# Optimization experiments

Measured on AMD Instinct MI355X. Metric: run time of the kernel, lower is better.

The kernel has to match this reference:

```python
import jax, jax.numpy as jnp
import numpy as np

DIM = 1024
NUM_HEADS = 16
HEAD_DIM = DIM // NUM_HEADS
MAX_LEN = 2048
ROPE_BASE = 10000.0


def _rope_tables(n, d, base=ROPE_BASE):
    inv_freq = 1.0 / (base ** (np.arange(0, d, 2, dtype=np.float32) / d))  # [d/2]
    t = np.arange(n, dtype=np.float32)
    freqs = np.outer(t, inv_freq)  # [n, d/2]
    return jnp.asarray(np.cos(freqs)), jnp.asarray(np.sin(freqs))


def _apply_rotary(x, cos, sin):
    # x: [B, H, N, D]; pairs are consecutive elements (2i, 2i+1)
    xe = x[..., 0::2]
    xo = x[..., 1::2]
    # cos/sin: [N, D/2] -> broadcast over B, H
    oe = xe * cos - xo * sin
    oo = xe * sin + xo * cos
    return jnp.stack([oe, oo], axis=-1).reshape(x.shape)


def setup_inputs() -> dict:
    key = jax.random.key(0)
    ks = jax.random.split(key, 11)
    B, T, S = 4, 2048, 2048
    sc = 1.0 / np.sqrt(DIM)
    inp = {
        "query": jax.random.normal(ks[0], (B, T, DIM), jnp.float32),
        "key": jax.random.normal(ks[1], (B, S, DIM), jnp.float32),
        "value": jax.random.normal(ks[2], (B, S, DIM), jnp.float32),
        "Wq": jax.random.normal(ks[3], (DIM, DIM), jnp.float32) * sc,
        "bq": jnp.zeros((DIM,), jnp.float32),
        "Wk": jax.random.normal(ks[4], (DIM, DIM), jnp.float32) * sc,
        "bk": jnp.zeros((DIM,), jnp.float32),
        "Wv": jax.random.normal(ks[5], (DIM, DIM), jnp.float32) * sc,
        "bv": jnp.zeros((DIM,), jnp.float32),
        "Wo": jax.random.normal(ks[6], (DIM, DIM), jnp.float32) * sc,
        "bo": jnp.zeros((DIM,), jnp.float32),
    }
    return inp


def reference(query, key, value, Wq, bq, Wk, bk, Wv, bv, Wo, bo):
    B, T, C = query.shape
    S = key.shape[1]
    H, D = NUM_HEADS, HEAD_DIM
    scale = D ** -0.5

    q = (query @ Wq + bq).reshape(B, T, H, D).transpose(0, 2, 1, 3)  # [B,H,T,D]
    k = (key @ Wk + bk).reshape(B, S, H, D).transpose(0, 2, 1, 3)    # [B,H,S,D]
    v = (value @ Wv + bv).reshape(B, S, H, D).transpose(0, 2, 1, 3)  # [B,H,S,D]

    cos, sin = _rope_tables(max(T, S), D)
    q = _apply_rotary(q, cos[:T], sin[:T])
    k = _apply_rotary(k, cos[:S], sin[:S])

    scores = jnp.einsum("bhtd,bhsd->bhts", q, k) * scale  # [B,H,T,S]
    causal = jnp.tril(jnp.ones((T, S), bool))
    scores = jnp.where(causal[None, None], scores, -jnp.inf)
    att = jax.nn.softmax(scores, axis=-1)

    out = jnp.einsum("bhts,bhsd->bhtd", att, v)  # [B,H,T,D]
    out = out.transpose(0, 2, 1, 3).reshape(B, T, C)
    return out @ Wo + bo
```

## Files before the change

kernel.cpp:

```cpp
#include <hip/hip_runtime.h>
#include <cstdint>
#include <math.h>

typedef __bf16 bf16_t;
typedef __bf16 bf16x8 __attribute__((ext_vector_type(8)));
typedef __bf16 bf16x4 __attribute__((ext_vector_type(4)));
typedef float f32x4 __attribute__((ext_vector_type(4)));

#define MFMA16(a, b, c) __builtin_amdgcn_mfma_f32_16x16x32_bf16((a), (b), (c), 0, 0, 0)

static constexpr int BATCH = 4;
static constexpr int SEQ = 2048;
static constexpr int DIMC = 1024;
static constexpr int NH = 16;
static constexpr int HD = 64;

__device__ __forceinline__ void async_copy16(void* lds, const void* g) {
    __builtin_amdgcn_global_load_lds(
        (const __attribute__((address_space(1))) void*)g,
        (__attribute__((address_space(3))) void*)lds, 16, 0, 0);
}

__device__ __forceinline__ float fast_exp2(float x) {
#if __has_builtin(__builtin_amdgcn_exp2f)
    return __builtin_amdgcn_exp2f(x);
#else
    return __expf(x * 0.6931471805599453f);
#endif
}

__global__ __launch_bounds__(256) void cvt3(const float* __restrict__ q,
                                            const float* __restrict__ k,
                                            const float* __restrict__ v,
                                            bf16_t* __restrict__ out) {
    const float* in = (blockIdx.y == 0) ? q : ((blockIdx.y == 1) ? k : v);
    bf16_t* o = out + (size_t)blockIdx.y * BATCH * SEQ * DIMC;
    const int i = blockIdx.x * 256 + threadIdx.x;
    const float4 f0 = ((const float4*)in)[i * 2];
    const float4 f1 = ((const float4*)in)[i * 2 + 1];
    bf16x8 vv;
    vv[0] = (bf16_t)f0.x; vv[1] = (bf16_t)f0.y; vv[2] = (bf16_t)f0.z; vv[3] = (bf16_t)f0.w;
    vv[4] = (bf16_t)f1.x; vv[5] = (bf16_t)f1.y; vv[6] = (bf16_t)f1.z; vv[7] = (bf16_t)f1.w;
    ((bf16x8*)o)[i] = vv;
}

__global__ __launch_bounds__(256) void transpose_cvt(const float* __restrict__ W0,
                                                     const float* __restrict__ W1,
                                                     const float* __restrict__ W2,
                                                     const float* __restrict__ W3,
                                                     bf16_t* __restrict__ out) {
    const float* Ws[4] = {W0, W1, W2, W3};
    const float* W = Ws[blockIdx.z];
    bf16_t* Wt = out + (size_t)blockIdx.z * DIMC * DIMC;
    __shared__ float tile[32][33];
    const int tx = threadIdx.x & 31;
    const int ty = threadIdx.x >> 5;
    const int x0 = blockIdx.x * 32;
    const int y0 = blockIdx.y * 32;
    #pragma unroll
    for (int j = ty; j < 32; j += 8)
        tile[j][tx] = W[(size_t)(y0 + j) * DIMC + x0 + tx];
    __syncthreads();
    #pragma unroll
    for (int j = ty; j < 32; j += 8)
        Wt[(size_t)(x0 + j) * DIMC + y0 + tx] = (bf16_t)tile[tx][j];
}

__global__ __launch_bounds__(256) void rope_tab(float* __restrict__ cosT, float* __restrict__ sinT) {
    const int idx = blockIdx.x * 256 + threadIdx.x;
    const int t = idx >> 5;
    const int p = idx & 31;
    const float inv = exp2f(-0.41524101186092029f * (float)p);
    const float ang = (float)t * inv;
    float s, c;
    sincosf(ang, &s, &c);
    cosT[idx] = c;
    sinT[idx] = s;
}

template <int MI>
__device__ __forceinline__ void gemm_core(const bf16_t* __restrict__ A,
                                          const bf16_t* __restrict__ Bt,
                                          const int row0, const int col0,
                                          bf16_t* As, bf16_t* Bs, const int tid,
                                          f32x4 (&acc)[MI][4]) {
    constexpr int ABUF = MI * 32 * 32;
    constexpr int BBUF = 256 * 32;
    constexpr int NT = DIMC / 32;
    const int wid = tid >> 6;
    const int lane = tid & 63;
    const int l15 = lane & 15;
    const int quad = lane >> 4;
    const int wr = wid >> 2;
    const int wc = wid & 3;
    const int rIn = lane >> 2;
    const int gW = ((lane & 3) ^ ((rIn & 3) ^ ((rIn >> 2) & 3))) * 8;
    const int fR = (l15 & 3) ^ ((l15 >> 2) & 3);

#define STAGE_TILE(bi, kt)                                                              \
    {                                                                                   \
        const int k0_ = (kt)*32;                                                        \
        bf16_t* as_ = As + (bi)*ABUF;                                                   \
        bf16_t* bs_ = Bs + (bi)*BBUF;                                                   \
        if constexpr (MI == 8) {                                                        \
            _Pragma("unroll") for (int ci = 0; ci < 2; ++ci) {                          \
                const int c = 2 * wid + ci;                                             \
                async_copy16(&as_[c * 512],                                             \
                             A + (size_t)(row0 + c * 16 + rIn) * DIMC + k0_ + gW);      \
            }                                                                           \
        } else {                                                                        \
            async_copy16(&as_[wid * 512],                                               \
                         A + (size_t)(row0 + wid * 16 + rIn) * DIMC + k0_ + gW);        \
        }                                                                               \
        _Pragma("unroll") for (int ci = 0; ci < 2; ++ci) {                              \
            const int c = 2 * wid + ci;                                                 \
            async_copy16(&bs_[c * 512],                                                 \
                         Bt + (size_t)(col0 + c * 16 + rIn) * DIMC + k0_ + gW);         \
        }                                                                               \
    }

    STAGE_TILE(0, 0)
    STAGE_TILE(1, 1)
    STAGE_TILE(2, 2)
    int rb = 0;
    for (int t = 0; t < NT; ++t) {
        const int rem = NT - 1 - t;
        if constexpr (MI == 8) {
            if (rem >= 2) asm volatile("s_waitcnt vmcnt(8)" ::: "memory");
            else if (rem == 1) asm volatile("s_waitcnt vmcnt(4)" ::: "memory");
            else asm volatile("s_waitcnt vmcnt(0)" ::: "memory");
        } else {
            if (rem >= 2) asm volatile("s_waitcnt vmcnt(6)" ::: "memory");
            else if (rem == 1) asm volatile("s_waitcnt vmcnt(3)" ::: "memory");
            else asm volatile("s_waitcnt vmcnt(0)" ::: "memory");
        }
        asm volatile("s_barrier" ::: "memory");
        if (t + 3 < NT) {
            int sb = rb + 3;
            if (sb >= 4) sb -= 4;
            STAGE_TILE(sb, t + 3)
        }
        const bf16_t* as = As + rb * ABUF;
        const bf16_t* bs = Bs + rb * BBUF;
        bf16x8 bfrag[4];
        #pragma unroll
        for (int ni = 0; ni < 4; ++ni)
            bfrag[ni] = *(const bf16x8*)&bs[(wc * 64 + ni * 16 + l15) * 32 + ((quad ^ fR) << 3)];
        bf16x8 afrag[MI];
        #pragma unroll
        for (int mi = 0; mi < MI; ++mi)
            afrag[mi] =
                *(const bf16x8*)&as[(wr * (MI * 16) + mi * 16 + l15) * 32 + ((quad ^ fR) << 3)];
        __builtin_amdgcn_s_setprio(1);
        #pragma unroll
        for (int mi = 0; mi < MI; ++mi)
            #pragma unroll
            for (int ni = 0; ni < 4; ++ni)
                acc[mi][ni] = MFMA16(afrag[mi], bfrag[ni], acc[mi][ni]);
        __builtin_amdgcn_s_setprio(0);
        rb = (rb + 1) & 3;
    }
#undef STAGE_TILE
}

__global__ __launch_bounds__(512, 2) void gemm_qkv(const bf16_t* __restrict__ Cb,
                                                   const bf16_t* __restrict__ Wt3,
                                                   const float* __restrict__ bq,
                                                   const float* __restrict__ bk,
                                                   const float* __restrict__ bv,
                                                   bf16_t* __restrict__ Qr,
                                                   bf16_t* __restrict__ Kr,
                                                   bf16_t* __restrict__ Vr,
                                                   const float* __restrict__ cosT,
                                                   const float* __restrict__ sinT) {
    __shared__ __align__(16) unsigned char smem[131072];
    bf16_t* As = (bf16_t*)smem;
    bf16_t* Bs = (bf16_t*)(smem + 65536);
    float* eps = (float*)smem;
    const int z = blockIdx.z;
    const bf16_t* A = Cb + (size_t)z * BATCH * SEQ * DIMC;
    const bf16_t* Bt = Wt3 + (size_t)z * DIMC * DIMC;
    const float* bias = (z == 0) ? bq : ((z == 1) ? bk : bv);
    bf16_t* outp = (z == 0) ? Qr : ((z == 1) ? Kr : Vr);
    const bool rope = (z < 2);
    const int tid = threadIdx.x;
    const int row0 = blockIdx.x * 256, col0 = blockIdx.y * 256;
    f32x4 acc[8][4] = {};
    gemm_core<8>(A, Bt, row0, col0, As, Bs, tid, acc);

    const int wid = tid >> 6;
    const int lane = tid & 63;
    const int l15 = lane & 15;
    const int quad = lane >> 4;
    const int wr = wid >> 2, wc = wid & 3;
    float bvl[4];
    #pragma unroll
    for (int ni = 0; ni < 4; ++ni) bvl[ni] = bias[col0 + wc * 64 + ni * 16 + l15];
    const int lr = tid >> 4;
    const int cg = tid & 15;
    const int c0 = cg * 16;
    const int h = (col0 + c0) >> 6;
    const int dbase = c0 & 63;
    const float osc = (z == 0) ? 0.18033688011112043f : 1.0f;
    #pragma unroll
    for (int p = 0; p < 8; ++p) {
        __syncthreads();
        #pragma unroll
        for (int ni = 0; ni < 4; ++ni)
            #pragma unroll
            for (int r = 0; r < 4; ++r)
                eps[(wr * 16 + quad * 4 + r) * 264 + wc * 64 + ni * 16 + l15] =
                    acc[p][ni][r] + bvl[ni];
        __syncthreads();
        const int grow = row0 + (lr >> 4) * 128 + p * 16 + (lr & 15);
        const int tq = grow & (SEQ - 1);
        const int bb = grow >> 11;
        float vals[16];
        #pragma unroll
        for (int q4 = 0; q4 < 4; ++q4) {
            f32x4 vv = *(const f32x4*)&eps[lr * 264 + c0 + q4 * 4];
            vals[q4 * 4 + 0] = vv[0]; vals[q4 * 4 + 1] = vv[1];
            vals[q4 * 4 + 2] = vv[2]; vals[q4 * 4 + 3] = vv[3];
        }
        bf16x8 o0, o1;
        if (rope) {
            const int pbase = tq * 32 + (dbase >> 1);
            const float4 cs0 = *(const float4*)&cosT[pbase];
            const float4 cs1 = *(const float4*)&cosT[pbase + 4];
            const float4 sn0 = *(const float4*)&sinT[pbase];
            const float4 sn1 = *(const float4*)&sinT[pbase + 4];
            const float cc[8] = {cs0.x, cs0.y, cs0.z, cs0.w, cs1.x, cs1.y, cs1.z, cs1.w};
            const float ss[8] = {sn0.x, sn0.y, sn0.z, sn0.w, sn1.x, sn1.y, sn1.z, sn1.w};
            #pragma unroll
            for (int i = 0; i < 8; ++i) {
                const float e = vals[2 * i], o = vals[2 * i + 1];
                const float oe = (e * cc[i] - o * ss[i]) * osc;
                const float oo = (e * ss[i] + o * cc[i]) * osc;
                if (i < 4) { o0[2 * i] = (bf16_t)oe; o0[2 * i + 1] = (bf16_t)oo; }
                else { o1[2 * (i - 4)] = (bf16_t)oe; o1[2 * (i - 4) + 1] = (bf16_t)oo; }
            }
        } else {
            #pragma unroll
            for (int i = 0; i < 8; ++i) o0[i] = (bf16_t)vals[i];
            #pragma unroll
            for (int i = 0; i < 8; ++i) o1[i] = (bf16_t)vals[8 + i];
        }
        bf16_t* dst = outp + (((size_t)bb * NH + h) * SEQ + tq) * HD + dbase;
        *(bf16x8*)dst = o0;
        *(bf16x8*)(dst + 8) = o1;
    }
}

__global__ __launch_bounds__(512, 2) void gemm_o(const bf16_t* __restrict__ A,
                                                 const bf16_t* __restrict__ Bt,
                                                 const float* __restrict__ bias,
                                                 float* __restrict__ out) {
    __shared__ __align__(16) unsigned char smem[98304];
    bf16_t* As = (bf16_t*)smem;
    bf16_t* Bs = (bf16_t*)(smem + 32768);
    const int tid = threadIdx.x;
    const int row0 = blockIdx.x * 128, col0 = blockIdx.y * 256;
    f32x4 acc[4][4] = {};
    gemm_core<4>(A, Bt, row0, col0, As, Bs, tid, acc);
    const int wid = tid >> 6;
    const int lane = tid & 63;
    const int l15 = lane & 15;
    const int quad = lane >> 4;
    const int wr = wid >> 2, wc = wid & 3;
    #pragma unroll
    for (int ni = 0; ni < 4; ++ni) {
        const int col = col0 + wc * 64 + ni * 16 + l15;
        const float bvl = bias[col];
        #pragma unroll
        for (int mi = 0; mi < 4; ++mi) {
            #pragma unroll
            for (int r = 0; r < 4; ++r) {
                const int row = row0 + wr * 64 + mi * 16 + quad * 4 + r;
                out[(size_t)row * DIMC + col] = acc[mi][ni][r] + bvl;
            }
        }
    }
}

__global__ __launch_bounds__(256) void attn_kernel(const bf16_t* __restrict__ Qr,
                                                   const bf16_t* __restrict__ Kr,
                                                   const bf16_t* __restrict__ Vr,
                                                   bf16_t* __restrict__ O) {
    __shared__ bf16_t Ks[2][64 * 64];
    __shared__ bf16_t Vt[2][64 * 72];
    __shared__ bf16_t Ps[4][32 * 72];
    const int tid = threadIdx.x;
    const int w = tid >> 6;
    const int lane = tid & 63;
    const int l15 = lane & 15;
    const int quad = lane >> 4;
    const int bh = blockIdx.x;
    const int b = bh >> 4, h = bh & 15;
    const bf16_t* Qb = Qr + (size_t)bh * SEQ * HD;
    const bf16_t* Kb = Kr + (size_t)bh * SEQ * HD;
    const bf16_t* Vb = Vr + (size_t)bh * SEQ * HD;

    bf16x8 ones;
    #pragma unroll
    for (int j8 = 0; j8 < 8; ++j8) ones[j8] = (bf16_t)1.0f;
    bf16x8 idB[2];
    #pragma unroll
    for (int ch = 0; ch < 2; ++ch)
        #pragma unroll
        for (int j8 = 0; j8 < 8; ++j8)
            idB[ch][j8] = (quad * 8 + j8 == ch * 16 + l15) ? (bf16_t)1.0f : (bf16_t)0.0f;

    const int sIn = lane >> 3;
    const int gK = ((lane & 7) ^ sIn) * 8;
    const int fK = (l15 & 7);

#define VTRANS(buf, a0, a1)                                                      \
    {                                                                            \
        _Pragma("unroll") for (int c = 0; c < 4; ++c) {                          \
            f32x4 zt = {};                                                       \
            f32x4 tv = MFMA16((c < 2) ? (a0) : (a1), idB[c & 1], zt);            \
            bf16x4 pkt;                                                          \
            _Pragma("unroll") for (int rr = 0; rr < 4; ++rr)                     \
                pkt[rr] = (bf16_t)tv[rr];                                        \
            *(bf16x4*)&Vt[buf][(c * 16 + l15) * 72 + w * 16 + quad * 4] = pkt;   \
        }                                                                        \
    }

    const int j = 15 - (int)blockIdx.y;
    const int q0 = j * 128;
    bf16x8 qa[2][2];
    #pragma unroll
    for (int mg = 0; mg < 2; ++mg)
        #pragma unroll
        for (int kc = 0; kc < 2; ++kc)
            qa[mg][kc] = *(const bf16x8*)(Qb + (size_t)(q0 + mg * 64 + w * 16 + l15) * HD +
                                          kc * 32 + quad * 8);
    f32x4 acco[2][4] = {};
    f32x4 accl[2] = {};
    const int nIter = 2 * j + 2;

    #pragma unroll
    for (int ci = 0; ci < 2; ++ci) {
        const int c = 2 * w + ci;
        async_copy16(&Ks[0][c * 512], Kb + (size_t)(c * 8 + sIn) * HD + gK);
    }
    {
        const bf16_t* vsrc = Vb + (size_t)(w * 16 + l15) * HD + quad * 8;
        bf16x8 pv0 = *(const bf16x8*)vsrc;
        bf16x8 pv1 = *(const bf16x8*)(vsrc + 32);
        VTRANS(0, pv0, pv1);
    }
    __syncthreads();

    int cur = 0;
    for (int it = 0; it < nIter; ++it) {
        const int nxt = cur ^ 1;
        const bool hn = (it + 1 < nIter);
        bf16x8 av0, av1;
        if (hn) {
            const int s1 = (it + 1) * 64;
            #pragma unroll
            for (int ci = 0; ci < 2; ++ci) {
                const int c = 2 * w + ci;
                async_copy16(&Ks[nxt][c * 512], Kb + (size_t)(s1 + c * 8 + sIn) * HD + gK);
            }
            const bf16_t* vsrc = Vb + (size_t)(s1 + w * 16 + l15) * HD + quad * 8;
            av0 = *(const bf16x8*)vsrc;
            av1 = *(const bf16x8*)(vsrc + 32);
        }
        bf16x8 kb[4][2];
        #pragma unroll
        for (int mt = 0; mt < 4; ++mt)
            #pragma unroll
            for (int kc = 0; kc < 2; ++kc)
                kb[mt][kc] = *(const bf16x8*)&Ks[cur][(mt * 16 + l15) * 64 +
                                                      (((kc * 4 + quad) ^ fK) << 3)];
        const bool skip0 = (it == 2 * j + 1);
        f32x4 zz[2][4];
        __builtin_amdgcn_s_setprio(1);
        #pragma unroll
        for (int mg = 0; mg < 2; ++mg) {
            if (mg == 0 && skip0) continue;
            #pragma unroll
            for (int mt = 0; mt < 4; ++mt) {
                f32x4 z = {};
                z = MFMA16(kb[mt][0], qa[mg][0], z);
                z = MFMA16(kb[mt][1], qa[mg][1], z);
                zz[mg][mt] = z;
            }
        }
        __builtin_amdgcn_s_setprio(0);
        #pragma unroll
        for (int mg = 0; mg < 2; ++mg) {
            if (mg == 0 && skip0) continue;
            const bool diag = (it == 2 * j + mg);
            #pragma unroll
            for (int mt = 0; mt < 4; ++mt) {
                bf16x4 pk;
                #pragma unroll
                for (int r = 0; r < 4; ++r) {
                    float v = zz[mg][mt][r];
                    if (diag && (mt * 16 + quad * 4 + r > w * 16 + l15)) v = -INFINITY;
                    pk[r] = (bf16_t)fast_exp2(v);
                }
                *(bf16x4*)&Ps[w][(mg * 16 + l15) * 72 + mt * 16 + quad * 4] = pk;
            }
        }
        asm volatile("s_waitcnt lgkmcnt(0)" ::: "memory");
        bf16x8 vb[4][2];
        #pragma unroll
        for (int dt = 0; dt < 4; ++dt)
            #pragma unroll
            for (int kc = 0; kc < 2; ++kc)
                vb[dt][kc] = *(const bf16x8*)&Vt[cur][(dt * 16 + l15) * 72 + kc * 32 + quad * 8];
        #pragma unroll
        for (int mg = 0; mg < 2; ++mg) {
            if (mg == 0 && skip0) continue;
            const bf16x8 pa0 = *(const bf16x8*)&Ps[w][(mg * 16 + l15) * 72 + quad * 8];
            const bf16x8 pa1 = *(const bf16x8*)&Ps[w][(mg * 16 + l15) * 72 + 32 + quad * 8];
            __builtin_amdgcn_s_setprio(1);
            #pragma unroll
            for (int dt = 0; dt < 4; ++dt) {
                acco[mg][dt] = MFMA16(pa0, vb[dt][0], acco[mg][dt]);
                acco[mg][dt] = MFMA16(pa1, vb[dt][1], acco[mg][dt]);
            }
            accl[mg] = MFMA16(pa0, ones, accl[mg]);
            accl[mg] = MFMA16(pa1, ones, accl[mg]);
            __builtin_amdgcn_s_setprio(0);
        }
        if (hn) VTRANS(nxt, av0, av1);
        __syncthreads();
        cur = nxt;
    }
    #pragma unroll
    for (int mg = 0; mg < 2; ++mg) {
        #pragma unroll
        for (int r = 0; r < 4; ++r) {
            const float inv = 1.0f / accl[mg][r];
            const int trow = q0 + mg * 64 + w * 16 + quad * 4 + r;
            bf16_t* orow = O + ((size_t)(b * SEQ + trow)) * DIMC + h * HD;
            #pragma unroll
            for (int dt = 0; dt < 4; ++dt)
                orow[dt * 16 + l15] = (bf16_t)(acco[mg][dt][r] * inv);
        }
    }
#undef VTRANS
}

extern "C" void kernel_launch(void* const* d_in, const int* in_sizes, int n_in,
                              void* d_out, int out_size, void* d_ws, size_t ws_size,
                              hipStream_t stream) {
    const float* query = (const float*)d_in[0];
    const float* key = (const float*)d_in[1];
    const float* value = (const float*)d_in[2];
    const float* Wq = (const float*)d_in[3];
    const float* bq = (const float*)d_in[4];
    const float* Wk = (const float*)d_in[5];
    const float* bk = (const float*)d_in[6];
    const float* Wv = (const float*)d_in[7];
    const float* bv = (const float*)d_in[8];
    const float* Wo = (const float*)d_in[9];
    const float* bo = (const float*)d_in[10];

    char* ws = (char*)d_ws;
    const size_t WT_BYTES = (size_t)DIMC * DIMC * sizeof(bf16_t);
    const size_t ACT_BYTES = (size_t)BATCH * SEQ * DIMC * sizeof(bf16_t);
    bf16_t* WT = (bf16_t*)ws;
    bf16_t* WoT = WT + 3 * (size_t)DIMC * DIMC;
    float* cosT = (float*)(ws + 4 * WT_BYTES);
    float* sinT = (float*)(ws + 4 * WT_BYTES + 262144);
    bf16_t* Cb = (bf16_t*)(ws + 4 * WT_BYTES + 2 * 262144);
    bf16_t* Qr = (bf16_t*)((char*)Cb + 3 * ACT_BYTES);
    bf16_t* Kr = (bf16_t*)((char*)Cb + 4 * ACT_BYTES);
    bf16_t* Vr = (bf16_t*)((char*)Cb + 5 * ACT_BYTES);
    bf16_t* Ob = Cb;

    transpose_cvt<<<dim3(32, 32, 4), 256, 0, stream>>>(Wq, Wk, Wv, Wo, WT);
    rope_tab<<<dim3(256), 256, 0, stream>>>(cosT, sinT);
    cvt3<<<dim3(4096, 3), 256, 0, stream>>>(query, key, value, Cb);
    gemm_qkv<<<dim3((BATCH * SEQ) / 256, DIMC / 256, 3), 512, 0, stream>>>(
        Cb, WT, bq, bk, bv, Qr, Kr, Vr, cosT, sinT);
    attn_kernel<<<dim3(BATCH * NH, 16), 256, 0, stream>>>(Qr, Kr, Vr, Ob);
    gemm_o<<<dim3((BATCH * SEQ) / 128, DIMC / 256), 512, 0, stream>>>(Ob, WoT, bo, (float*)d_out);
}
```

Measured before the change: 335.5 us.

## Restructure GEMM main loop into interleaved load/MFMA phases with split staging

Replaces the templated GEMM core with two specialized cores whose K-loop is split into four phases. Each phase interleaves LDS fragment reads, one slice of async global->LDS staging, and a block of MFMAs, separated by barriers. Prefetch depth drops from three tiles to two. The aim is to overlap memory issue with MFMA work and keep fewer fragments live in registers, at the cost of many more barriers per iteration and less prefetch lead.

```diff
diff --git a/kernel.cpp b/kernel.cpp
--- a/kernel.cpp
+++ b/kernel.cpp
@@ -78,14 +78,14 @@
     sinT[idx] = s;
 }
 
-template <int MI>
-__device__ __forceinline__ void gemm_core(const bf16_t* __restrict__ A,
-                                          const bf16_t* __restrict__ Bt,
-                                          const int row0, const int col0,
-                                          bf16_t* As, bf16_t* Bs, const int tid,
-                                          f32x4 (&acc)[MI][4]) {
-    constexpr int ABUF = MI * 32 * 32;
-    constexpr int BBUF = 256 * 32;
+
+__device__ __forceinline__ void gemm_core8(const bf16_t* __restrict__ A,
+                                           const bf16_t* __restrict__ Bt,
+                                           const int row0, const int col0,
+                                           bf16_t* As, bf16_t* Bs, const int tid,
+                                           f32x4 (&acc)[8][4]) {
+    constexpr int ABUF = 8192;
+    constexpr int BBUF = 8192;
     constexpr int NT = DIMC / 32;
     const int wid = tid >> 6;
     const int lane = tid & 63;
@@ -96,71 +96,178 @@
     const int rIn = lane >> 2;
     const int gW = ((lane & 3) ^ ((rIn & 3) ^ ((rIn >> 2) & 3))) * 8;
     const int fR = (l15 & 3) ^ ((l15 >> 2) & 3);
-
-#define STAGE_TILE(bi, kt)                                                              \
-    {                                                                                   \
-        const int k0_ = (kt)*32;                                                        \
-        bf16_t* as_ = As + (bi)*ABUF;                                                   \
-        bf16_t* bs_ = Bs + (bi)*BBUF;                                                   \
-        if constexpr (MI == 8) {                                                        \
-            _Pragma("unroll") for (int ci = 0; ci < 2; ++ci) {                          \
-                const int c = 2 * wid + ci;                                             \
-                async_copy16(&as_[c * 512],                                             \
-                             A + (size_t)(row0 + c * 16 + rIn) * DIMC + k0_ + gW);      \
-            }                                                                           \
-        } else {                                                                        \
-            async_copy16(&as_[wid * 512],                                               \
-                         A + (size_t)(row0 + wid * 16 + rIn) * DIMC + k0_ + gW);        \
-        }                                                                               \
-        _Pragma("unroll") for (int ci = 0; ci < 2; ++ci) {                              \
-            const int c = 2 * wid + ci;                                                 \
-            async_copy16(&bs_[c * 512],                                                 \
-                         Bt + (size_t)(col0 + c * 16 + rIn) * DIMC + k0_ + gW);         \
-        }                                                                               \
-    }
-
-    STAGE_TILE(0, 0)
-    STAGE_TILE(1, 1)
-    STAGE_TILE(2, 2)
-    int rb = 0;
+    const int rdoff = (quad ^ fR) << 3;
+
+#define STG_A8(bi, kt, h)                                                     \
+    async_copy16(As + (bi)*ABUF + (h)*4096 + wid * 512,                       \
+                 A + (size_t)(row0 + (h)*128 + wid * 16 + rIn) * DIMC +       \
+                     (kt)*32 + gW);
+#define STG_B8(bi, kt, h)                                                     \
+    async_copy16(Bs + (bi)*BBUF + (h)*4096 + wid * 512,                       \
+                 Bt + (size_t)(col0 + (h)*128 + wid * 16 + rIn) * DIMC +      \
+                     (kt)*32 + gW);
+
+    STG_A8(0, 0, 0) STG_A8(0, 0, 1) STG_B8(0, 0, 0) STG_B8(0, 0, 1)
+    STG_A8(1, 1, 0) STG_A8(1, 1, 1) STG_B8(1, 1, 0) STG_B8(1, 1, 1)
+    asm volatile("s_waitcnt vmcnt(4)" ::: "memory");
+    __builtin_amdgcn_s_barrier();
+
+    #pragma unroll 1
     for (int t = 0; t < NT; ++t) {
-        const int rem = NT - 1 - t;
-        if constexpr (MI == 8) {
-            if (rem >= 2) asm volatile("s_waitcnt vmcnt(8)" ::: "memory");
-            else if (rem == 1) asm volatile("s_waitcnt vmcnt(4)" ::: "memory");
-            else asm volatile("s_waitcnt vmcnt(0)" ::: "memory");
-        } else {
-            if (rem >= 2) asm volatile("s_waitcnt vmcnt(6)" ::: "memory");
-            else if (rem == 1) asm volatile("s_waitcnt vmcnt(3)" ::: "memory");
-            else asm volatile("s_waitcnt vmcnt(0)" ::: "memory");
-        }
-        asm volatile("s_barrier" ::: "memory");
-        if (t + 3 < NT) {
-            int sb = rb + 3;
-            if (sb >= 4) sb -= 4;
-            STAGE_TILE(sb, t + 3)
-        }
+        const int rb = t & 3;
+        const int sb = (t + 2) & 3;
+        const int kt2 = t + 2;
+        const bool st = kt2 < NT;
         const bf16_t* as = As + rb * ABUF;
         const bf16_t* bs = Bs + rb * BBUF;
-        bf16x8 bfrag[4];
-        #pragma unroll
-        for (int ni = 0; ni < 4; ++ni)
-            bfrag[ni] = *(const bf16x8*)&bs[(wc * 64 + ni * 16 + l15) * 32 + ((quad ^ fR) << 3)];
-        bf16x8 afrag[MI];
-        #pragma unroll
-        for (int mi = 0; mi < MI; ++mi)
-            afrag[mi] =
-                *(const bf16x8*)&as[(wr * (MI * 16) + mi * 16 + l15) * 32 + ((quad ^ fR) << 3)];
-        __builtin_amdgcn_s_setprio(1);
-        #pragma unroll
-        for (int mi = 0; mi < MI; ++mi)
-            #pragma unroll
-            for (int ni = 0; ni < 4; ++ni)
-                acc[mi][ni] = MFMA16(afrag[mi], bfrag[ni], acc[mi][ni]);
-        __builtin_amdgcn_s_setprio(0);
-        rb = (rb + 1) & 3;
-    }
-#undef STAGE_TILE
+        bf16x8 af[4], bf[4];
+        #pragma unroll
+        for (int i = 0; i < 4; ++i)
+            af[i] = *(const bf16x8*)&as[(wr * 128 + i * 16 + l15) * 32 + rdoff];
+        #pragma unroll
+        for (int i = 0; i < 2; ++i)
+            bf[i] = *(const bf16x8*)&bs[(wc * 64 + i * 16 + l15) * 32 + rdoff];
+        if (st) STG_A8(sb, kt2, 0)
+        __builtin_amdgcn_s_barrier();
+        asm volatile("s_waitcnt lgkmcnt(0)" ::: "memory");
+        __builtin_amdgcn_sched_barrier(0);
+        __builtin_amdgcn_s_setprio(1);
+        #pragma unroll
+        for (int mi = 0; mi < 4; ++mi)
+            #pragma unroll
+            for (int ni = 0; ni < 2; ++ni)
+                acc[mi][ni] = MFMA16(af[mi], bf[ni], acc[mi][ni]);
+        __builtin_amdgcn_s_setprio(0);
+        __builtin_amdgcn_s_barrier();
+        #pragma unroll
+        for (int i = 2; i < 4; ++i)
+            bf[i] = *(const bf16x8*)&bs[(wc * 64 + i * 16 + l15) * 32 + rdoff];
+        if (st) STG_A8(sb, kt2, 1)
+        __builtin_amdgcn_s_barrier();
+        asm volatile("s_waitcnt lgkmcnt(0)" ::: "memory");
+        __builtin_amdgcn_sched_barrier(0);
+        __builtin_amdgcn_s_setprio(1);
+        #pragma unroll
+        for (int mi = 0; mi < 4; ++mi)
+            #pragma unroll
+            for (int ni = 2; ni < 4; ++ni)
+                acc[mi][ni] = MFMA16(af[mi], bf[ni], acc[mi][ni]);
+        __builtin_amdgcn_s_setprio(0);
+        __builtin_amdgcn_s_barrier();
+        #pragma unroll
+        for (int i = 0; i < 4; ++i)
+            af[i] = *(const bf16x8*)&as[(wr * 128 + (4 + i) * 16 + l15) * 32 + rdoff];
+        if (st) STG_B8(sb, kt2, 0)
+        __builtin_amdgcn_s_barrier();
+        asm volatile("s_waitcnt lgkmcnt(0)" ::: "memory");
+        __builtin_amdgcn_sched_barrier(0);
+        __builtin_amdgcn_s_setprio(1);
+        #pragma unroll
+        for (int mi = 0; mi < 4; ++mi)
+            #pragma unroll
+            for (int ni = 0; ni < 2; ++ni)
+                acc[4 + mi][ni] = MFMA16(af[mi], bf[ni], acc[4 + mi][ni]);
+        __builtin_amdgcn_s_setprio(0);
+        __builtin_amdgcn_s_barrier();
+        if (st) STG_B8(sb, kt2, 1)
+        __builtin_amdgcn_s_setprio(1);
+        #pragma unroll
+        for (int mi = 0; mi < 4; ++mi)
+            #pragma unroll
+            for (int ni = 2; ni < 4; ++ni)
+                acc[4 + mi][ni] = MFMA16(af[mi], bf[ni], acc[4 + mi][ni]);
+        __builtin_amdgcn_s_setprio(0);
+        if (t < NT - 2)
+            asm volatile("s_waitcnt vmcnt(4)" ::: "memory");
+        else
+            asm volatile("s_waitcnt vmcnt(0)" ::: "memory");
+        __builtin_amdgcn_s_barrier();
+    }
+#undef STG_A8
+#undef STG_B8
+}
+
+__device__ __forceinline__ void gemm_core4(const bf16_t* __restrict__ A,
+                                           const bf16_t* __restrict__ Bt,
+                                           const int row0, const int col0,
+                                           bf16_t* As, bf16_t* Bs, const int tid,
+                                           f32x4 (&acc)[4][4]) {
+    constexpr int ABUF = 4096;
+    constexpr int BBUF = 8192;
+    constexpr int NT = DIMC / 32;
+    const int wid = tid >> 6;
+    const int lane = tid & 63;
+    const int l15 = lane & 15;
+    const int quad = lane >> 4;
+    const int wr = wid >> 2;
+    const int wc = wid & 3;
+    const int rIn = lane >> 2;
+    const int gW = ((lane & 3) ^ ((rIn & 3) ^ ((rIn >> 2) & 3))) * 8;
+    const int fR = (l15 & 3) ^ ((l15 >> 2) & 3);
+    const int rdoff = (quad ^ fR) << 3;
+
+#define STG_A4(bi, kt)                                                        \
+    async_copy16(As + (bi)*ABUF + wid * 512,                                  \
+                 A + (size_t)(row0 + wid * 16 + rIn) * DIMC + (kt)*32 + gW);
+#define STG_B4(bi, kt, h)                                                     \
+    async_copy16(Bs + (bi)*BBUF + (h)*4096 + wid * 512,                       \
+                 Bt + (size_t)(col0 + (h)*128 + wid * 16 + rIn) * DIMC +      \
+                     (kt)*32 + gW);
+
+    STG_A4(0, 0) STG_B4(0, 0, 0) STG_B4(0, 0, 1)
+    STG_A4(1, 1) STG_B4(1, 1, 0) STG_B4(1, 1, 1)
+    asm volatile("s_waitcnt vmcnt(3)" ::: "memory");
+    __builtin_amdgcn_s_barrier();
+
+    #pragma unroll 1
+    for (int t = 0; t < NT; ++t) {
+        const int rb = t & 3;
+        const int sb = (t + 2) & 3;
+        const int kt2 = t + 2;
+        const bool st = kt2 < NT;
+        const bf16_t* as = As + rb * ABUF;
+        const bf16_t* bs = Bs + rb * BBUF;
+        bf16x8 af[4], bf[4];
+        #pragma unroll
+        for (int i = 0; i < 4; ++i)
+            af[i] = *(const bf16x8*)&as[(wr * 64 + i * 16 + l15) * 32 + rdoff];
+        #pragma unroll
+        for (int i = 0; i < 2; ++i)
+            bf[i] = *(const bf16x8*)&bs[(wc * 64 + i * 16 + l15) * 32 + rdoff];
+        if (st) { STG_A4(sb, kt2) STG_B4(sb, kt2, 0) }
+        __builtin_amdgcn_s_barrier();
+        asm volatile("s_waitcnt lgkmcnt(0)" ::: "memory");
+        __builtin_amdgcn_sched_barrier(0);
+        __builtin_amdgcn_s_setprio(1);
+        #pragma unroll
+        for (int mi = 0; mi < 4; ++mi)
+            #pragma unroll
+            for (int ni = 0; ni < 2; ++ni)
+                acc[mi][ni] = MFMA16(af[mi], bf[ni], acc[mi][ni]);
+        __builtin_amdgcn_s_setprio(0);
+        __builtin_amdgcn_s_barrier();
+        #pragma unroll
+        for (int i = 2; i < 4; ++i)
+            bf[i] = *(const bf16x8*)&bs[(wc * 64 + i * 16 + l15) * 32 + rdoff];
+        if (st) STG_B4(sb, kt2, 1)
+        __builtin_amdgcn_s_barrier();
+        asm volatile("s_waitcnt lgkmcnt(0)" ::: "memory");
+        __builtin_amdgcn_sched_barrier(0);
+        __builtin_amdgcn_s_setprio(1);
+        #pragma unroll
+        for (int mi = 0; mi < 4; ++mi)
+            #pragma unroll
+            for (int ni = 2; ni < 4; ++ni)
+                acc[mi][ni] = MFMA16(af[mi], bf[ni], acc[mi][ni]);
+        __builtin_amdgcn_s_setprio(0);
+        if (t < NT - 2)
+            asm volatile("s_waitcnt vmcnt(3)" ::: "memory");
+        else
+            asm volatile("s_waitcnt vmcnt(0)" ::: "memory");
+        __builtin_amdgcn_s_barrier();
+    }
+#undef STG_A4
+#undef STG_B4
 }
 
 __global__ __launch_bounds__(512, 2) void gemm_qkv(const bf16_t* __restrict__ Cb,
@@ -186,7 +293,7 @@
     const int tid = threadIdx.x;
     const int row0 = blockIdx.x * 256, col0 = blockIdx.y * 256;
     f32x4 acc[8][4] = {};
-    gemm_core<8>(A, Bt, row0, col0, As, Bs, tid, acc);
+    gemm_core8(A, Bt, row0, col0, As, Bs, tid, acc);
 
     const int wid = tid >> 6;
     const int lane = tid & 63;
@@ -261,7 +368,7 @@
     const int tid = threadIdx.x;
     const int row0 = blockIdx.x * 128, col0 = blockIdx.y * 256;
     f32x4 acc[4][4] = {};
-    gemm_core<4>(A, Bt, row0, col0, As, Bs, tid, acc);
+    gemm_core4(A, Bt, row0, col0, As, Bs, tid, acc);
     const int wid = tid >> 6;
     const int lane = tid & 63;
     const int l15 = lane & 15;
```

After: 335.1 us. No clear change (-0.1%).
